# Kernel optimization log

Measured on AMD Instinct MI355X. Metric: run time of the kernel, lower is better.

## Reference

```python
import jax, jax.numpy as jnp
import numpy as np

N, D_IN, D_H, D_OUT = 65536, 256, 256, 128
E, TOP_K = 16, 2


def setup_inputs() -> dict:
    key = jax.random.key(0)
    ks = jax.random.split(key, 16)
    s = 0.05
    inp = {
        'x': jax.random.normal(ks[0], (N, D_IN), jnp.float32),
        'W0': jax.random.normal(ks[1], (D_IN, D_H), jnp.float32) * s,
        'b0': jnp.zeros((D_H,), jnp.float32),
        'Wg1': jax.random.normal(ks[2], (D_H, E), jnp.float32) * s,
        'bg1': jnp.zeros((E,), jnp.float32),
        'We1': jax.random.normal(ks[3], (E, D_H, D_H), jnp.float32) * s,
        'be1': jnp.zeros((E, D_H), jnp.float32),
        'Wg2': jax.random.normal(ks[4], (D_H, E), jnp.float32) * s,
        'bg2': jnp.zeros((E,), jnp.float32),
        'We2': jax.random.normal(ks[5], (E, D_H, D_H), jnp.float32) * s,
        'be2': jnp.zeros((E, D_H), jnp.float32),
        'Wf': jax.random.normal(ks[6], (D_H, D_OUT), jnp.float32) * s,
        'bf': jnp.zeros((D_OUT,), jnp.float32),
    }
    return inp


def _moe_layer(h, Wg, bg, We, be):
    # naive gate: logits over experts, top-k, renormalized softmax of top-k vals
    logits = h @ Wg + bg                      # [N, E]
    gate_full = jax.nn.softmax(logits, axis=-1)  # returned 'gate' for std stat
    vals, idx = jax.lax.top_k(logits, TOP_K)  # [N, k]
    scores = jax.nn.softmax(vals, axis=-1)    # [N, k]
    # scatter top-k scores into dense combine weights [N, E]
    cw = (jax.nn.one_hot(idx, E, dtype=h.dtype) * scores[..., None]).sum(axis=1)
    # grouped GEMM expressed as masked per-expert GEMMs (E is small, fixed)
    y = jnp.zeros((h.shape[0], We.shape[-1]), h.dtype)
    for e in range(E):
        y = y + cw[:, e:e + 1] * (h @ We[e] + be[e])
    # torch.std defaults to unbiased (ddof=1)
    gate_std_mean = jnp.std(gate_full, axis=1, ddof=1).mean()
    return y, gate_std_mean


def reference(x, W0, b0, Wg1, bg1, We1, be1, Wg2, bg2, We2, be2, Wf, bf):
    h = jax.nn.relu(x @ W0 + b0)
    h, g1 = _moe_layer(h, Wg1, bg1, We1, be1)
    h = jax.nn.relu(h)
    h, g2 = _moe_layer(h, Wg2, bg2, We2, be2)
    h = jax.nn.relu(h)
    out = h @ Wf + bf
    gate_std_means_mean = (g1 + g2) * 0.5
    return out, gate_std_means_mean
```

## Files before the change

kernel.cpp:

```cpp
#include <hip/hip_runtime.h>
#include <math.h>

#define NT 65536
#define DH 256
#define DO 128
#define NE 16

struct RInfo { int e1, e2; float s1, s2; };

typedef __attribute__((ext_vector_type(8))) short bh8;
typedef __attribute__((ext_vector_type(4))) float fx4;

static __device__ __forceinline__ short f2bf(float f) {
    union { float f; unsigned u; } v; v.f = f;
    return (short)((v.u + 0x7FFFu + ((v.u >> 16) & 1u)) >> 16);
}

template<bool RELU>
__global__ __launch_bounds__(256)
void gemm_dense(const float* __restrict__ A, const float* __restrict__ B,
                const float* __restrict__ bias, float* __restrict__ C,
                int ncols)
{
    __shared__ float As[128][24];
    __shared__ float Bs[16][132];
    const int tid = threadIdx.x;
    const int tx = tid & 15, ty = tid >> 4;
    const int rowBase = blockIdx.x * 128;
    const int colBase = blockIdx.y * 128;

    const int ra0 = tid >> 2, ga = tid & 3;
    const int kb0 = tid >> 5, cb = tid & 31;

    float acc[8][8];
#pragma unroll
    for (int i = 0; i < 8; ++i)
#pragma unroll
        for (int j = 0; j < 8; ++j) acc[i][j] = 0.f;

    for (int kt = 0; kt < DH; kt += 16) {
        *reinterpret_cast<float4*>(&As[ra0][ga * 4]) =
            *reinterpret_cast<const float4*>(&A[(size_t)(rowBase + ra0) * DH + kt + ga * 4]);
        *reinterpret_cast<float4*>(&As[ra0 + 64][ga * 4]) =
            *reinterpret_cast<const float4*>(&A[(size_t)(rowBase + ra0 + 64) * DH + kt + ga * 4]);
        *reinterpret_cast<float4*>(&Bs[kb0][cb * 4]) =
            *reinterpret_cast<const float4*>(&B[(size_t)(kt + kb0) * ncols + colBase + cb * 4]);
        *reinterpret_cast<float4*>(&Bs[kb0 + 8][cb * 4]) =
            *reinterpret_cast<const float4*>(&B[(size_t)(kt + kb0 + 8) * ncols + colBase + cb * 4]);
        __syncthreads();
#pragma unroll
        for (int k4 = 0; k4 < 16; k4 += 4) {
            alignas(16) float ar[8][4];
#pragma unroll
            for (int i = 0; i < 8; ++i)
                *reinterpret_cast<float4*>(ar[i]) =
                    *reinterpret_cast<const float4*>(&As[ty * 8 + i][k4]);
#pragma unroll
            for (int kk = 0; kk < 4; ++kk) {
                alignas(16) float br[8];
                *reinterpret_cast<float4*>(&br[0]) =
                    *reinterpret_cast<const float4*>(&Bs[k4 + kk][tx * 8]);
                *reinterpret_cast<float4*>(&br[4]) =
                    *reinterpret_cast<const float4*>(&Bs[k4 + kk][tx * 8 + 4]);
#pragma unroll
                for (int i = 0; i < 8; ++i) {
                    const float a = ar[i][kk];
#pragma unroll
                    for (int j = 0; j < 8; ++j)
                        acc[i][j] = fmaf(a, br[j], acc[i][j]);
                }
            }
        }
        __syncthreads();
    }
    alignas(16) float bb[8];
#pragma unroll
    for (int j = 0; j < 8; ++j) bb[j] = bias[colBase + tx * 8 + j];
#pragma unroll
    for (int i = 0; i < 8; ++i) {
        const size_t row = rowBase + ty * 8 + i;
        alignas(16) float o[8];
#pragma unroll
        for (int j = 0; j < 8; ++j) {
            float v = acc[i][j] + bb[j];
            if (RELU) v = fmaxf(v, 0.f);
            o[j] = v;
        }
        float* p = &C[row * (size_t)ncols + colBase + tx * 8];
        *reinterpret_cast<float4*>(p)     = *reinterpret_cast<float4*>(&o[0]);
        *reinterpret_cast<float4*>(p + 4) = *reinterpret_cast<float4*>(&o[4]);
    }
}

__global__ __launch_bounds__(256)
void gate_kernel(const float* __restrict__ H, const float* __restrict__ Wg,
                 const float* __restrict__ bg, RInfo* __restrict__ info,
                 float* gsum)
{
    __shared__ float wgs[256][17];
    __shared__ float hs[16][260];
    __shared__ float lg[16][17];
    __shared__ float sbg[16];
    __shared__ float sds[16];
    const int tid = threadIdx.x;
    const int rowBase = blockIdx.x * 16;

#pragma unroll
    for (int i = 0; i < 16; ++i) {
        const int idx = tid + 256 * i;
        wgs[idx >> 4][idx & 15] = Wg[idx];
    }
    if (tid < 16) sbg[tid] = bg[tid];
#pragma unroll
    for (int it = 0; it < 4; ++it) {
        const int flat = (tid + 256 * it) * 4;
        const int r = flat >> 8, k = flat & 255;
        *reinterpret_cast<float4*>(&hs[r][k]) =
            *reinterpret_cast<const float4*>(&H[(size_t)(rowBase + r) * DH + k]);
    }
    __syncthreads();
    {
        const int r = tid >> 4, e = tid & 15;
        float acc = 0.f;
#pragma unroll 8
        for (int k = 0; k < 256; ++k) acc = fmaf(hs[r][k], wgs[k][e], acc);
        lg[r][e] = acc + sbg[e];
    }
    __syncthreads();
    if (tid < 16) {
        const int row = rowBase + tid;
        float l[16];
#pragma unroll
        for (int i = 0; i < 16; ++i) l[i] = lg[tid][i];
        int i1 = 0; float v1 = l[0];
#pragma unroll
        for (int i = 1; i < 16; ++i) if (l[i] > v1) { v1 = l[i]; i1 = i; }
        int i2 = -1; float v2 = -INFINITY;
#pragma unroll
        for (int i = 0; i < 16; ++i) if (i != i1 && l[i] > v2) { v2 = l[i]; i2 = i; }
        const float t = expf(v2 - v1);
        const float s1 = 1.f / (1.f + t);
        const float s2 = t / (1.f + t);
        float p[16]; float S = 0.f;
#pragma unroll
        for (int i = 0; i < 16; ++i) { p[i] = expf(l[i] - v1); S += p[i]; }
        const float inv = 1.f / S;
        float sq = 0.f;
#pragma unroll
        for (int i = 0; i < 16; ++i) { const float q = p[i] * inv; sq = fmaf(q, q, sq); }
        const float var = (sq - 1.0f / 16.0f) * (1.0f / 15.0f);
        const float sd = sqrtf(fmaxf(var, 0.f));

        RInfo ri; ri.e1 = i1; ri.e2 = i2; ri.s1 = s1; ri.s2 = s2;
        info[row] = ri;
        sds[tid] = sd;
    }
    __syncthreads();
    if (tid == 0) {
        float s = 0.f;
#pragma unroll
        for (int i = 0; i < 16; ++i) s += sds[i];
        atomicAdd(gsum, s);
    }
}

__global__ void zero_gsum(float* gsum)
{
    if (threadIdx.x < 2) gsum[threadIdx.x] = 0.f;
}

__global__ __launch_bounds__(256)
void count_kernel(const RInfo* __restrict__ info, int* __restrict__ bc0,
                  int* __restrict__ bc1)
{
    __shared__ int h0[NE], h1[NE];
    const int tid = threadIdx.x, b = blockIdx.x;
    if (tid < NE) { h0[tid] = 0; h1[tid] = 0; }
    __syncthreads();
    const RInfo ri = info[b * 256 + tid];
    atomicAdd(&h0[ri.e1], 1);
    atomicAdd(&h1[ri.e2], 1);
    __syncthreads();
    if (tid < NE) {
        bc0[tid * 256 + b] = h0[tid];
        bc1[tid * 256 + b] = h1[tid];
    }
}

__global__ void scan2_kernel(const int* __restrict__ bc0, const int* __restrict__ bc1,
                             int* cnt0, int* cnt1, int* off0, int* off1,
                             int* __restrict__ bo0, int* __restrict__ bo1)
{
    __shared__ int tot0[NE], tot1[NE], base0[NE], base1[NE];
    const int t = threadIdx.x;
    if (t < NE) {
        int s = 0;
        for (int b = 0; b < 256; ++b) s += bc0[t * 256 + b];
        tot0[t] = s; cnt0[t] = s;
    } else if (t < 2 * NE) {
        const int e = t - NE;
        int s = 0;
        for (int b = 0; b < 256; ++b) s += bc1[e * 256 + b];
        tot1[e] = s; cnt1[e] = s;
    }
    __syncthreads();
    if (t == 0) { int a = 0; for (int e = 0; e < NE; ++e) { base0[e] = a; off0[e] = a; a += tot0[e]; } }
    if (t == 1) { int a = 0; for (int e = 0; e < NE; ++e) { base1[e] = a; off1[e] = a; a += tot1[e]; } }
    __syncthreads();
    if (t < NE) {
        int run = base0[t];
        for (int b = 0; b < 256; ++b) { bo0[t * 256 + b] = run; run += bc0[t * 256 + b]; }
    } else if (t < 2 * NE) {
        const int e = t - NE;
        int run = base1[e];
        for (int b = 0; b < 256; ++b) { bo1[e * 256 + b] = run; run += bc1[e * 256 + b]; }
    }
}

__global__ __launch_bounds__(256)
void scatter2_kernel(const RInfo* __restrict__ info, const int* __restrict__ bo0,
                     const int* __restrict__ bo1, int* __restrict__ l0,
                     int* __restrict__ l1)
{
    __shared__ int h0[NE], h1[NE];
    const int tid = threadIdx.x, b = blockIdx.x;
    if (tid < NE) { h0[tid] = 0; h1[tid] = 0; }
    __syncthreads();
    const int r = b * 256 + tid;
    const RInfo ri = info[r];
    const int p0 = atomicAdd(&h0[ri.e1], 1);
    const int p1 = atomicAdd(&h1[ri.e2], 1);
    l0[bo0[ri.e1 * 256 + b] + p0] = r;
    l1[bo1[ri.e2 * 256 + b] + p1] = r;
}

template<int SLOT>
__global__ __launch_bounds__(256)
void gemm_expert(const float* __restrict__ Hin, const float* __restrict__ We,
                 const float* __restrict__ be, const RInfo* __restrict__ info,
                 const int* __restrict__ list, const int* __restrict__ cnts,
                 const int* __restrict__ offs, float* __restrict__ P,
                 short* __restrict__ Ybf)
{
    __shared__ float As[128][24];
    __shared__ float Bs[16][132];
    __shared__ int   rs[128];
    __shared__ float ss[128];

    int c = blockIdx.x, e;
    int cnt = 0;
    for (e = 0; e < NE; ++e) {
        cnt = cnts[e];
        const int nch = (cnt + 127) >> 7;
        if (c < nch) break;
        c -= nch;
    }
    if (e >= NE) return;
    const int m = min(128, cnt - c * 128);
    const int base = offs[e] + c * 128;
    const int tid = threadIdx.x;
    const int tx = tid & 15, ty = tid >> 4;
    const int colBase = blockIdx.y * 128;

    if (tid < 128) {
        const int g = list[base + min(tid, m - 1)];
        rs[tid] = g;
        const RInfo ri = info[g];
        ss[tid] = (SLOT == 0) ? ri.s1 : ri.s2;
    }
    __syncthreads();

    const float* B = We + (size_t)e * DH * DH;
    const int ra0 = tid >> 2, ga = tid & 3;
    const int kb0 = tid >> 5, cb = tid & 31;
    const size_t arow0 = (size_t)rs[ra0] * DH;
    const size_t arow1 = (size_t)rs[ra0 + 64] * DH;

    float acc[8][8];
#pragma unroll
    for (int i = 0; i < 8; ++i)
#pragma unroll
        for (int j = 0; j < 8; ++j) acc[i][j] = 0.f;

    for (int kt = 0; kt < DH; kt += 16) {
        *reinterpret_cast<float4*>(&As[ra0][ga * 4]) =
            *reinterpret_cast<const float4*>(&Hin[arow0 + kt + ga * 4]);
        *reinterpret_cast<float4*>(&As[ra0 + 64][ga * 4]) =
            *reinterpret_cast<const float4*>(&Hin[arow1 + kt + ga * 4]);
        *reinterpret_cast<float4*>(&Bs[kb0][cb * 4]) =
            *reinterpret_cast<const float4*>(&B[(size_t)(kt + kb0) * DH + colBase + cb * 4]);
        *reinterpret_cast<float4*>(&Bs[kb0 + 8][cb * 4]) =
            *reinterpret_cast<const float4*>(&B[(size_t)(kt + kb0 + 8) * DH + colBase + cb * 4]);
        __syncthreads();
#pragma unroll
        for (int k4 = 0; k4 < 16; k4 += 4) {
            alignas(16) float ar[8][4];
#pragma unroll
            for (int i = 0; i < 8; ++i)
                *reinterpret_cast<float4*>(ar[i]) =
                    *reinterpret_cast<const float4*>(&As[ty * 8 + i][k4]);
#pragma unroll
            for (int kk = 0; kk < 4; ++kk) {
                alignas(16) float br[8];
                *reinterpret_cast<float4*>(&br[0]) =
                    *reinterpret_cast<const float4*>(&Bs[k4 + kk][tx * 8]);
                *reinterpret_cast<float4*>(&br[4]) =
                    *reinterpret_cast<const float4*>(&Bs[k4 + kk][tx * 8 + 4]);
#pragma unroll
                for (int i = 0; i < 8; ++i) {
                    const float a = ar[i][kk];
#pragma unroll
                    for (int j = 0; j < 8; ++j)
                        acc[i][j] = fmaf(a, br[j], acc[i][j]);
                }
            }
        }
        __syncthreads();
    }

    alignas(16) float bb[8];
#pragma unroll
    for (int j = 0; j < 8; ++j) bb[j] = be[(size_t)e * DH + colBase + tx * 8 + j];
#pragma unroll
    for (int i = 0; i < 8; ++i) {
        const int rl = ty * 8 + i;
        if (rl < m) {
            const int g = rs[rl];
            const float s = ss[rl];
            alignas(16) float o[8];
#pragma unroll
            for (int j = 0; j < 8; ++j) o[j] = s * (acc[i][j] + bb[j]);
            float* pp = &P[(size_t)g * DH + colBase + tx * 8];
            if (SLOT == 0) {
                *reinterpret_cast<float4*>(pp)     = *reinterpret_cast<float4*>(&o[0]);
                *reinterpret_cast<float4*>(pp + 4) = *reinterpret_cast<float4*>(&o[4]);
            } else {
                const float4 p0 = *reinterpret_cast<const float4*>(pp);
                const float4 p1 = *reinterpret_cast<const float4*>(pp + 4);
                alignas(16) float h[8];
                h[0] = fmaxf(o[0] + p0.x, 0.f); h[1] = fmaxf(o[1] + p0.y, 0.f);
                h[2] = fmaxf(o[2] + p0.z, 0.f); h[3] = fmaxf(o[3] + p0.w, 0.f);
                h[4] = fmaxf(o[4] + p1.x, 0.f); h[5] = fmaxf(o[5] + p1.y, 0.f);
                h[6] = fmaxf(o[6] + p1.z, 0.f); h[7] = fmaxf(o[7] + p1.w, 0.f);
                *reinterpret_cast<float4*>(pp)     = *reinterpret_cast<float4*>(&h[0]);
                *reinterpret_cast<float4*>(pp + 4) = *reinterpret_cast<float4*>(&h[4]);
                if (Ybf) {
                    bh8 yb;
#pragma unroll
                    for (int j = 0; j < 8; ++j) yb[j] = f2bf(h[j]);
                    *reinterpret_cast<bh8*>(&Ybf[(size_t)g * DH + colBase + tx * 8]) = yb;
                }
            }
        }
    }
}

__global__ __launch_bounds__(256)
void transp_bf16(const float* __restrict__ W, short* __restrict__ WT,
                 int K, int N)
{
    __shared__ float t[32][33];
    const int k0 = blockIdx.x * 32, n0 = blockIdx.y * 32;
    const size_t off = (size_t)blockIdx.z * K * N;
    const int c = threadIdx.x & 31, r8 = threadIdx.x >> 5;
#pragma unroll
    for (int it = 0; it < 4; ++it) {
        const int r = r8 + it * 8;
        t[r][c] = W[off + (size_t)(k0 + r) * N + n0 + c];
    }
    __syncthreads();
#pragma unroll
    for (int it = 0; it < 4; ++it) {
        const int r = r8 + it * 8;
        WT[off + (size_t)(n0 + r) * K + k0 + c] = f2bf(t[c][r]);
    }
}

template<int SLOT, int BFA>
__global__ __launch_bounds__(256)
void gemm_expert_bf16(const float* __restrict__ Yf, const short* __restrict__ Abf,
                      const short* __restrict__ WeT,
                      const float* __restrict__ be, const RInfo* __restrict__ info,
                      const int* __restrict__ list, const int* __restrict__ cnts,
                      const int* __restrict__ offs, float* __restrict__ P,
                      short* __restrict__ Hbf)
{
    __shared__ bh8 As8[512];
    __shared__ bh8 Bs8[512];
    __shared__ int   rs[128];
    __shared__ float ss[128];

    int c = blockIdx.x, e;
    int cnt = 0;
    for (e = 0; e < NE; ++e) {
        cnt = cnts[e];
        const int nch = (cnt + 127) >> 7;
        if (c < nch) break;
        c -= nch;
    }
    if (e >= NE) return;
    const int m = min(128, cnt - c * 128);
    const int base = offs[e] + c * 128;
    const int tid = threadIdx.x;

    if (tid < 128) {
        const int g = list[base + min(tid, m - 1)];
        rs[tid] = g;
        const RInfo ri = info[g];
        ss[tid] = (SLOT == 0) ? ri.s1 : ri.s2;
    }
    __syncthreads();

    const int colBase = blockIdx.y * 128;
    const int lane = tid & 63, wave = tid >> 6;
    const int wr = wave >> 1, wc = wave & 1;
    const short* Bw = WeT + (size_t)e * DH * DH;

    fx4 acc[4][4];
    const fx4 z = {0.f, 0.f, 0.f, 0.f};
#pragma unroll
    for (int i = 0; i < 4; ++i)
#pragma unroll
        for (int j = 0; j < 4; ++j) acc[i][j] = z;

    const int d0 = tid, d1 = tid + 256;
    const int ar0 = d0 >> 2, ak0 = d0 & 3;
    const int ar1 = d1 >> 2, ak1 = d1 & 3;
    const int g0 = ar0 * 4 + (ak0 ^ ((ar0 >> 1) & 3));
    const int g1 = ar1 * 4 + (ak1 ^ ((ar1 >> 1) & 3));
    const size_t arow0 = (size_t)rs[ar0] * DH, arow1 = (size_t)rs[ar1] * DH;
    const size_t brow0 = (size_t)(colBase + ar0) * DH, brow1 = (size_t)(colBase + ar1) * DH;

    for (int kt = 0; kt < DH; kt += 32) {
        if (BFA) {
            As8[g0] = *reinterpret_cast<const bh8*>(&Abf[arow0 + kt + ak0 * 8]);
            As8[g1] = *reinterpret_cast<const bh8*>(&Abf[arow1 + kt + ak1 * 8]);
        } else {
            const float* s0 = &Yf[arow0 + kt + ak0 * 8];
            const float4 f0 = *reinterpret_cast<const float4*>(s0);
            const float4 f1 = *reinterpret_cast<const float4*>(s0 + 4);
            bh8 v;
            v[0]=f2bf(f0.x); v[1]=f2bf(f0.y); v[2]=f2bf(f0.z); v[3]=f2bf(f0.w);
            v[4]=f2bf(f1.x); v[5]=f2bf(f1.y); v[6]=f2bf(f1.z); v[7]=f2bf(f1.w);
            As8[g0] = v;
            const float* s1 = &Yf[arow1 + kt + ak1 * 8];
            const float4 f2 = *reinterpret_cast<const float4*>(s1);
            const float4 f3 = *reinterpret_cast<const float4*>(s1 + 4);
            bh8 w;
            w[0]=f2bf(f2.x); w[1]=f2bf(f2.y); w[2]=f2bf(f2.z); w[3]=f2bf(f2.w);
            w[4]=f2bf(f3.x); w[5]=f2bf(f3.y); w[6]=f2bf(f3.z); w[7]=f2bf(f3.w);
            As8[g1] = w;
        }
        {
            Bs8[g0] = *reinterpret_cast<const bh8*>(&Bw[brow0 + kt + ak0 * 8]);
            Bs8[g1] = *reinterpret_cast<const bh8*>(&Bw[brow1 + kt + ak1 * 8]);
        }
        __syncthreads();
        const int kq = lane >> 4, lm = lane & 15;
        bh8 af[4], bfr[4];
#pragma unroll
        for (int i = 0; i < 4; ++i) {
            const int rl = wr * 64 + i * 16 + lm;
            af[i] = As8[rl * 4 + (kq ^ ((rl >> 1) & 3))];
            const int cl = wc * 64 + i * 16 + lm;
            bfr[i] = Bs8[cl * 4 + (kq ^ ((cl >> 1) & 3))];
        }
#pragma unroll
        for (int i = 0; i < 4; ++i)
#pragma unroll
            for (int j = 0; j < 4; ++j)
                acc[i][j] = __builtin_amdgcn_mfma_f32_16x16x32_bf16(
                    af[i], bfr[j], acc[i][j], 0, 0, 0);
        __syncthreads();
    }

    const int rq = lane >> 4, lm = lane & 15;
#pragma unroll
    for (int i = 0; i < 4; ++i) {
#pragma unroll
        for (int j = 0; j < 4; ++j) {
            const int rl = wr * 64 + i * 16 + rq * 4 + j;
            if (rl < m) {
                const int g = rs[rl];
                const float s = ss[rl];
#pragma unroll
                for (int nf = 0; nf < 4; ++nf) {
                    const int cl = colBase + wc * 64 + nf * 16 + lm;
                    float* pp = &P[(size_t)g * DH + cl];
                    const float o = s * (acc[i][nf][j] + be[(size_t)e * DH + cl]);
                    if (SLOT == 0) {
                        *pp = o;
                    } else {
                        const float v = fmaxf(*pp + o, 0.f);
                        if (BFA) Hbf[(size_t)g * DH + cl] = f2bf(v);
                        else     *pp = v;
                    }
                }
            }
        }
    }
}

template<int BFA>
__global__ __launch_bounds__(256)
void gemm_final_bf16(const float* __restrict__ Hf, const short* __restrict__ Habf,
                     const short* __restrict__ WT,
                     const float* __restrict__ bias, float* __restrict__ C,
                     const float* gsum, float* scalar_out)
{
    __shared__ bh8 As8[512];
    __shared__ bh8 Bs8[512];
    const int tid = threadIdx.x;
    const int rowBase = blockIdx.x * 128;

    if (blockIdx.x == 0 && tid == 0)
        *scalar_out = (gsum[0] + gsum[1]) * (0.5f / (float)NT);

    const int lane = tid & 63, wave = tid >> 6;
    const int wr = wave >> 1, wc = wave & 1;

    fx4 acc[4][4];
    const fx4 z = {0.f, 0.f, 0.f, 0.f};
#pragma unroll
    for (int i = 0; i < 4; ++i)
#pragma unroll
        for (int j = 0; j < 4; ++j) acc[i][j] = z;

    const int d0 = tid, d1 = tid + 256;
    const int ar0 = d0 >> 2, ak0 = d0 & 3;
    const int ar1 = d1 >> 2, ak1 = d1 & 3;
    const int g0 = ar0 * 4 + (ak0 ^ ((ar0 >> 1) & 3));
    const int g1 = ar1 * 4 + (ak1 ^ ((ar1 >> 1) & 3));
    const size_t arow0 = (size_t)(rowBase + ar0) * DH, arow1 = (size_t)(rowBase + ar1) * DH;
    const size_t brow0 = (size_t)ar0 * DH, brow1 = (size_t)ar1 * DH;

    for (int kt = 0; kt < DH; kt += 32) {
        if (BFA) {
            As8[g0] = *reinterpret_cast<const bh8*>(&Habf[arow0 + kt + ak0 * 8]);
            As8[g1] = *reinterpret_cast<const bh8*>(&Habf[arow1 + kt + ak1 * 8]);
        } else {
            const float* s0 = &Hf[arow0 + kt + ak0 * 8];
            const float4 f0 = *reinterpret_cast<const float4*>(s0);
            const float4 f1 = *reinterpret_cast<const float4*>(s0 + 4);
            bh8 v;
            v[0]=f2bf(f0.x); v[1]=f2bf(f0.y); v[2]=f2bf(f0.z); v[3]=f2bf(f0.w);
            v[4]=f2bf(f1.x); v[5]=f2bf(f1.y); v[6]=f2bf(f1.z); v[7]=f2bf(f1.w);
            As8[g0] = v;
            const float* s1 = &Hf[arow1 + kt + ak1 * 8];
            const float4 f2 = *reinterpret_cast<const float4*>(s1);
            const float4 f3 = *reinterpret_cast<const float4*>(s1 + 4);
            bh8 w;
            w[0]=f2bf(f2.x); w[1]=f2bf(f2.y); w[2]=f2bf(f2.z); w[3]=f2bf(f2.w);
            w[4]=f2bf(f3.x); w[5]=f2bf(f3.y); w[6]=f2bf(f3.z); w[7]=f2bf(f3.w);
            As8[g1] = w;
        }
        {
            Bs8[g0] = *reinterpret_cast<const bh8*>(&WT[brow0 + kt + ak0 * 8]);
            Bs8[g1] = *reinterpret_cast<const bh8*>(&WT[brow1 + kt + ak1 * 8]);
        }
        __syncthreads();
        const int kq = lane >> 4, lm = lane & 15;
        bh8 af[4], bfr[4];
#pragma unroll
        for (int i = 0; i < 4; ++i) {
            const int rl = wr * 64 + i * 16 + lm;
            af[i] = As8[rl * 4 + (kq ^ ((rl >> 1) & 3))];
            const int cl = wc * 64 + i * 16 + lm;
            bfr[i] = Bs8[cl * 4 + (kq ^ ((cl >> 1) & 3))];
        }
#pragma unroll
        for (int i = 0; i < 4; ++i)
#pragma unroll
            for (int j = 0; j < 4; ++j)
                acc[i][j] = __builtin_amdgcn_mfma_f32_16x16x32_bf16(
                    af[i], bfr[j], acc[i][j], 0, 0, 0);
        __syncthreads();
    }

    const int rq = lane >> 4, lm = lane & 15;
#pragma unroll
    for (int i = 0; i < 4; ++i) {
#pragma unroll
        for (int j = 0; j < 4; ++j) {
            const int rl = rowBase + wr * 64 + i * 16 + rq * 4 + j;
#pragma unroll
            for (int nf = 0; nf < 4; ++nf) {
                const int cl = wc * 64 + nf * 16 + lm;
                C[(size_t)rl * DO + cl] = acc[i][nf][j] + bias[cl];
            }
        }
    }
}

extern "C" void kernel_launch(void* const* d_in, const int* in_sizes, int n_in,
                              void* d_out, int out_size, void* d_ws, size_t ws_size,
                              hipStream_t stream)
{
    const float* x   = (const float*)d_in[0];
    const float* W0  = (const float*)d_in[1];
    const float* b0  = (const float*)d_in[2];
    const float* Wg1 = (const float*)d_in[3];
    const float* bg1 = (const float*)d_in[4];
    const float* We1 = (const float*)d_in[5];
    const float* be1 = (const float*)d_in[6];
    const float* Wg2 = (const float*)d_in[7];
    const float* bg2 = (const float*)d_in[8];
    const float* We2 = (const float*)d_in[9];
    const float* be2 = (const float*)d_in[10];
    const float* Wf  = (const float*)d_in[11];
    const float* bf  = (const float*)d_in[12];
    float* out = (float*)d_out;

    char* w = (char*)d_ws;
    float* H    = (float*)w; w += (size_t)NT * DH * 4;
    float* Y    = (float*)w; w += (size_t)NT * DH * 4;
    RInfo* info = (RInfo*)w; w += (size_t)NT * sizeof(RInfo);
    int* l0   = (int*)w; w += (size_t)NT * 4;
    int* l1   = (int*)w; w += (size_t)NT * 4;
    int* bc0  = (int*)w; w += NE * 256 * 4;
    int* bc1  = (int*)w; w += NE * 256 * 4;
    int* bo0  = (int*)w; w += NE * 256 * 4;
    int* bo1  = (int*)w; w += NE * 256 * 4;
    int* cnt0 = (int*)w; w += 64;
    int* cnt1 = (int*)w; w += 64;
    int* off0 = (int*)w; w += 64;
    int* off1 = (int*)w; w += 64;
    float* gsum = (float*)w; w += 64;
    short* WeT = (short*)w; w += (size_t)NE * DH * DH * 2;
    short* WfT = (short*)w; w += (size_t)DH * DO * 2;
    short* Ybf = (short*)w; w += (size_t)NT * DH * 2;
    const bool roomy = (size_t)(w - (char*)d_ws) <= ws_size;
    short* Hbf = (short*)Y;

    const int MAXCH = NT / 128 + NE;

    zero_gsum<<<dim3(1), dim3(64), 0, stream>>>(gsum);
    transp_bf16<<<dim3(8, 8, 16), dim3(256), 0, stream>>>(We2, WeT, DH, DH);
    transp_bf16<<<dim3(8, 4, 1),  dim3(256), 0, stream>>>(Wf,  WfT, DH, DO);

    gemm_dense<true><<<dim3(NT / 128, 2), dim3(256), 0, stream>>>(x, W0, b0, H, DH);

    gate_kernel<<<dim3(NT / 16), dim3(256), 0, stream>>>(H, Wg1, bg1, info, &gsum[0]);
    count_kernel<<<dim3(NT / 256), dim3(256), 0, stream>>>(info, bc0, bc1);
    scan2_kernel<<<dim3(1), dim3(64), 0, stream>>>(bc0, bc1, cnt0, cnt1, off0, off1, bo0, bo1);
    scatter2_kernel<<<dim3(NT / 256), dim3(256), 0, stream>>>(info, bo0, bo1, l0, l1);
    gemm_expert<0><<<dim3(MAXCH, 2), dim3(256), 0, stream>>>(H, We1, be1, info, l0, cnt0, off0, Y, nullptr);
    gemm_expert<1><<<dim3(MAXCH, 2), dim3(256), 0, stream>>>(H, We1, be1, info, l1, cnt1, off1, Y,
                                                             roomy ? Ybf : nullptr);

    gate_kernel<<<dim3(NT / 16), dim3(256), 0, stream>>>(Y, Wg2, bg2, info, &gsum[1]);
    count_kernel<<<dim3(NT / 256), dim3(256), 0, stream>>>(info, bc0, bc1);
    scan2_kernel<<<dim3(1), dim3(64), 0, stream>>>(bc0, bc1, cnt0, cnt1, off0, off1, bo0, bo1);
    scatter2_kernel<<<dim3(NT / 256), dim3(256), 0, stream>>>(info, bo0, bo1, l0, l1);
    if (roomy) {
        gemm_expert_bf16<0,1><<<dim3(MAXCH, 2), dim3(256), 0, stream>>>(Y, Ybf, WeT, be2, info, l0, cnt0, off0, H, nullptr);
        gemm_expert_bf16<1,1><<<dim3(MAXCH, 2), dim3(256), 0, stream>>>(Y, Ybf, WeT, be2, info, l1, cnt1, off1, H, Hbf);
        gemm_final_bf16<1><<<dim3(NT / 128), dim3(256), 0, stream>>>(H, Hbf, WfT, bf, out, gsum, out + (size_t)NT * DO);
    } else {
        gemm_expert_bf16<0,0><<<dim3(MAXCH, 2), dim3(256), 0, stream>>>(Y, nullptr, WeT, be2, info, l0, cnt0, off0, H, nullptr);
        gemm_expert_bf16<1,0><<<dim3(MAXCH, 2), dim3(256), 0, stream>>>(Y, nullptr, WeT, be2, info, l1, cnt1, off1, H, nullptr);
        gemm_final_bf16<0><<<dim3(NT / 128), dim3(256), 0, stream>>>(H, nullptr, WfT, bf, out, gsum, out + (size_t)NT * DO);
    }
}
```

Measured before the change: 630.0 us.

## Fuse expert counting into gate kernel, deepen fp32 GEMM K-tile, remap expert chunks

Folds the per-block expert histogram into the gate kernel using shared atomics plus global atomicAdd into zeroed bucket arrays. This removes the separate count kernel launch and its reread of routing info, and the scan kernel now re-zeros the buckets after use. The fp32 dense and expert GEMMs switch from a K-tile of 16 to 32, halving the number of barrier/load iterations at the cost of more shared memory. Expert GEMM blocks are remapped so that consecutive block IDs are strided across chunks (8 x 66), and the gate weight load is vectorised.

```diff
diff --git a/kernel.cpp b/kernel.cpp
--- a/kernel.cpp
+++ b/kernel.cpp
@@ -5,6 +5,8 @@
 #define DH 256
 #define DO 128
 #define NE 16
+#define MAXCH 528
+#define CPX 66
 
 struct RInfo { int e1, e2; float s1, s2; };
 
@@ -22,34 +24,41 @@
                 const float* __restrict__ bias, float* __restrict__ C,
                 int ncols)
 {
-    __shared__ float As[128][24];
-    __shared__ float Bs[16][132];
+    __shared__ float As[128][36];
+    __shared__ float Bs[32][132];
     const int tid = threadIdx.x;
     const int tx = tid & 15, ty = tid >> 4;
     const int rowBase = blockIdx.x * 128;
     const int colBase = blockIdx.y * 128;
 
-    const int ra0 = tid >> 2, ga = tid & 3;
-    const int kb0 = tid >> 5, cb = tid & 31;
-
     float acc[8][8];
 #pragma unroll
     for (int i = 0; i < 8; ++i)
 #pragma unroll
         for (int j = 0; j < 8; ++j) acc[i][j] = 0.f;
 
-    for (int kt = 0; kt < DH; kt += 16) {
-        *reinterpret_cast<float4*>(&As[ra0][ga * 4]) =
-            *reinterpret_cast<const float4*>(&A[(size_t)(rowBase + ra0) * DH + kt + ga * 4]);
-        *reinterpret_cast<float4*>(&As[ra0 + 64][ga * 4]) =
-            *reinterpret_cast<const float4*>(&A[(size_t)(rowBase + ra0 + 64) * DH + kt + ga * 4]);
-        *reinterpret_cast<float4*>(&Bs[kb0][cb * 4]) =
-            *reinterpret_cast<const float4*>(&B[(size_t)(kt + kb0) * ncols + colBase + cb * 4]);
-        *reinterpret_cast<float4*>(&Bs[kb0 + 8][cb * 4]) =
-            *reinterpret_cast<const float4*>(&B[(size_t)(kt + kb0 + 8) * ncols + colBase + cb * 4]);
-        __syncthreads();
-#pragma unroll
-        for (int k4 = 0; k4 < 16; k4 += 4) {
+    for (int kt = 0; kt < DH; kt += 32) {
+        {
+            const int r = tid >> 3, k4 = (tid & 7) << 2;
+#pragma unroll
+            for (int it = 0; it < 4; ++it) {
+                const float4 v = *reinterpret_cast<const float4*>(
+                    &A[(size_t)(rowBase + r + 32 * it) * DH + kt + k4]);
+                *reinterpret_cast<float4*>(&As[r + 32 * it][k4]) = v;
+            }
+        }
+        {
+            const int kr = tid >> 5, c4 = (tid & 31) << 2;
+#pragma unroll
+            for (int it = 0; it < 4; ++it) {
+                const float4 v = *reinterpret_cast<const float4*>(
+                    &B[(size_t)(kt + kr + 8 * it) * ncols + colBase + c4]);
+                *reinterpret_cast<float4*>(&Bs[kr + 8 * it][c4]) = v;
+            }
+        }
+        __syncthreads();
+#pragma unroll
+        for (int k4 = 0; k4 < 32; k4 += 4) {
             alignas(16) float ar[8][4];
 #pragma unroll
             for (int i = 0; i < 8; ++i)
@@ -95,22 +104,25 @@
 __global__ __launch_bounds__(256)
 void gate_kernel(const float* __restrict__ H, const float* __restrict__ Wg,
                  const float* __restrict__ bg, RInfo* __restrict__ info,
-                 float* gsum)
-{
-    __shared__ float wgs[256][17];
+                 float* gsum, int* __restrict__ bc0, int* __restrict__ bc1)
+{
+    __shared__ float wgs[256][20];
     __shared__ float hs[16][260];
     __shared__ float lg[16][17];
     __shared__ float sbg[16];
     __shared__ float sds[16];
+    __shared__ int hh0[NE], hh1[NE];
     const int tid = threadIdx.x;
     const int rowBase = blockIdx.x * 16;
 
 #pragma unroll
-    for (int i = 0; i < 16; ++i) {
-        const int idx = tid + 256 * i;
-        wgs[idx >> 4][idx & 15] = Wg[idx];
-    }
-    if (tid < 16) sbg[tid] = bg[tid];
+    for (int it = 0; it < 4; ++it) {
+        const int flat = (tid + 256 * it) * 4;
+        const int k = flat >> 4, e4 = flat & 15;
+        *reinterpret_cast<float4*>(&wgs[k][e4]) =
+            *reinterpret_cast<const float4*>(&Wg[flat]);
+    }
+    if (tid < 16) { sbg[tid] = bg[tid]; hh0[tid] = 0; hh1[tid] = 0; }
 #pragma unroll
     for (int it = 0; it < 4; ++it) {
         const int flat = (tid + 256 * it) * 4;
@@ -154,6 +166,8 @@
         RInfo ri; ri.e1 = i1; ri.e2 = i2; ri.s1 = s1; ri.s2 = s2;
         info[row] = ri;
         sds[tid] = sd;
+        atomicAdd(&hh0[i1], 1);
+        atomicAdd(&hh1[i2], 1);
     }
     __syncthreads();
     if (tid == 0) {
@@ -162,32 +176,21 @@
         for (int i = 0; i < 16; ++i) s += sds[i];
         atomicAdd(gsum, s);
     }
-}
-
-__global__ void zero_gsum(float* gsum)
-{
-    if (threadIdx.x < 2) gsum[threadIdx.x] = 0.f;
-}
-
-__global__ __launch_bounds__(256)
-void count_kernel(const RInfo* __restrict__ info, int* __restrict__ bc0,
-                  int* __restrict__ bc1)
-{
-    __shared__ int h0[NE], h1[NE];
-    const int tid = threadIdx.x, b = blockIdx.x;
-    if (tid < NE) { h0[tid] = 0; h1[tid] = 0; }
-    __syncthreads();
-    const RInfo ri = info[b * 256 + tid];
-    atomicAdd(&h0[ri.e1], 1);
-    atomicAdd(&h1[ri.e2], 1);
-    __syncthreads();
-    if (tid < NE) {
-        bc0[tid * 256 + b] = h0[tid];
-        bc1[tid * 256 + b] = h1[tid];
-    }
-}
-
-__global__ void scan2_kernel(const int* __restrict__ bc0, const int* __restrict__ bc1,
+    if (tid < 16) {
+        const int b = blockIdx.x >> 4;
+        if (hh0[tid]) atomicAdd(&bc0[tid * 256 + b], hh0[tid]);
+        if (hh1[tid]) atomicAdd(&bc1[tid * 256 + b], hh1[tid]);
+    }
+}
+
+__global__ void zero_meta(int* bc0, int* bc1, float* gsum)
+{
+    const int idx = blockIdx.x * 256 + threadIdx.x;
+    bc0[idx] = 0; bc1[idx] = 0;
+    if (idx < 2) gsum[idx] = 0.f;
+}
+
+__global__ void scan2_kernel(int* __restrict__ bc0, int* __restrict__ bc1,
                              int* cnt0, int* cnt1, int* off0, int* off1,
                              int* __restrict__ bo0, int* __restrict__ bo1)
 {
@@ -215,6 +218,8 @@
         int run = base1[e];
         for (int b = 0; b < 256; ++b) { bo1[e * 256 + b] = run; run += bc1[e * 256 + b]; }
     }
+    __syncthreads();
+    for (int i = t; i < NE * 256; i += 64) { bc0[i] = 0; bc1[i] = 0; }
 }
 
 __global__ __launch_bounds__(256)
@@ -242,12 +247,13 @@
                  const int* __restrict__ offs, float* __restrict__ P,
                  short* __restrict__ Ybf)
 {
-    __shared__ float As[128][24];
-    __shared__ float Bs[16][132];
+    __shared__ float As[128][36];
+    __shared__ float Bs[32][132];
     __shared__ int   rs[128];
     __shared__ float ss[128];
 
-    int c = blockIdx.x, e;
+    int c = (blockIdx.x & 7) * CPX + (blockIdx.x >> 3);
+    int e;
     int cnt = 0;
     for (e = 0; e < NE; ++e) {
         cnt = cnts[e];
@@ -271,10 +277,6 @@
     __syncthreads();
 
     const float* B = We + (size_t)e * DH * DH;
-    const int ra0 = tid >> 2, ga = tid & 3;
-    const int kb0 = tid >> 5, cb = tid & 31;
-    const size_t arow0 = (size_t)rs[ra0] * DH;
-    const size_t arow1 = (size_t)rs[ra0 + 64] * DH;
 
     float acc[8][8];
 #pragma unroll
@@ -282,18 +284,29 @@
 #pragma unroll
         for (int j = 0; j < 8; ++j) acc[i][j] = 0.f;
 
-    for (int kt = 0; kt < DH; kt += 16) {
-        *reinterpret_cast<float4*>(&As[ra0][ga * 4]) =
-            *reinterpret_cast<const float4*>(&Hin[arow0 + kt + ga * 4]);
-        *reinterpret_cast<float4*>(&As[ra0 + 64][ga * 4]) =
-            *reinterpret_cast<const float4*>(&Hin[arow1 + kt + ga * 4]);
-        *reinterpret_cast<float4*>(&Bs[kb0][cb * 4]) =
-            *reinterpret_cast<const float4*>(&B[(size_t)(kt + kb0) * DH + colBase + cb * 4]);
-        *reinterpret_cast<float4*>(&Bs[kb0 + 8][cb * 4]) =
-            *reinterpret_cast<const float4*>(&B[(size_t)(kt + kb0 + 8) * DH + colBase + cb * 4]);
-        __syncthreads();
-#pragma unroll
-        for (int k4 = 0; k4 < 16; k4 += 4) {
+    for (int kt = 0; kt < DH; kt += 32) {
+        {
+            const int r = tid >> 3, k4 = (tid & 7) << 2;
+#pragma unroll
+            for (int it = 0; it < 4; ++it) {
+                const int g = rs[r + 32 * it];
+                const float4 v = *reinterpret_cast<const float4*>(
+                    &Hin[(size_t)g * DH + kt + k4]);
+                *reinterpret_cast<float4*>(&As[r + 32 * it][k4]) = v;
+            }
+        }
+        {
+            const int kr = tid >> 5, c4 = (tid & 31) << 2;
+#pragma unroll
+            for (int it = 0; it < 4; ++it) {
+                const float4 v = *reinterpret_cast<const float4*>(
+                    &B[(size_t)(kt + kr + 8 * it) * DH + colBase + c4]);
+                *reinterpret_cast<float4*>(&Bs[kr + 8 * it][c4]) = v;
+            }
+        }
+        __syncthreads();
+#pragma unroll
+        for (int k4 = 0; k4 < 32; k4 += 4) {
             alignas(16) float ar[8][4];
 #pragma unroll
             for (int i = 0; i < 8; ++i)
@@ -390,7 +403,8 @@
     __shared__ int   rs[128];
     __shared__ float ss[128];
 
-    int c = blockIdx.x, e;
+    int c = (blockIdx.x & 7) * CPX + (blockIdx.x >> 3);
+    int e;
     int cnt = 0;
     for (e = 0; e < NE; ++e) {
         cnt = cnts[e];
@@ -632,24 +646,20 @@
     const bool roomy = (size_t)(w - (char*)d_ws) <= ws_size;
     short* Hbf = (short*)Y;
 
-    const int MAXCH = NT / 128 + NE;
-
-    zero_gsum<<<dim3(1), dim3(64), 0, stream>>>(gsum);
+    zero_meta<<<dim3(16), dim3(256), 0, stream>>>(bc0, bc1, gsum);
     transp_bf16<<<dim3(8, 8, 16), dim3(256), 0, stream>>>(We2, WeT, DH, DH);
     transp_bf16<<<dim3(8, 4, 1),  dim3(256), 0, stream>>>(Wf,  WfT, DH, DO);
 
     gemm_dense<true><<<dim3(NT / 128, 2), dim3(256), 0, stream>>>(x, W0, b0, H, DH);
 
-    gate_kernel<<<dim3(NT / 16), dim3(256), 0, stream>>>(H, Wg1, bg1, info, &gsum[0]);
-    count_kernel<<<dim3(NT / 256), dim3(256), 0, stream>>>(info, bc0, bc1);
+    gate_kernel<<<dim3(NT / 16), dim3(256), 0, stream>>>(H, Wg1, bg1, info, &gsum[0], bc0, bc1);
     scan2_kernel<<<dim3(1), dim3(64), 0, stream>>>(bc0, bc1, cnt0, cnt1, off0, off1, bo0, bo1);
     scatter2_kernel<<<dim3(NT / 256), dim3(256), 0, stream>>>(info, bo0, bo1, l0, l1);
     gemm_expert<0><<<dim3(MAXCH, 2), dim3(256), 0, stream>>>(H, We1, be1, info, l0, cnt0, off0, Y, nullptr);
     gemm_expert<1><<<dim3(MAXCH, 2), dim3(256), 0, stream>>>(H, We1, be1, info, l1, cnt1, off1, Y,
                                                              roomy ? Ybf : nullptr);
 
-    gate_kernel<<<dim3(NT / 16), dim3(256), 0, stream>>>(Y, Wg2, bg2, info, &gsum[1]);
-    count_kernel<<<dim3(NT / 256), dim3(256), 0, stream>>>(info, bc0, bc1);
+    gate_kernel<<<dim3(NT / 16), dim3(256), 0, stream>>>(Y, Wg2, bg2, info, &gsum[1], bc0, bc1);
     scan2_kernel<<<dim3(1), dim3(64), 0, stream>>>(bc0, bc1, cnt0, cnt1, off0, off1, bo0, bo1);
     scatter2_kernel<<<dim3(NT / 256), dim3(256), 0, stream>>>(info, bo0, bo1, l0, l1);
     if (roomy) {
```

Measured after the change: 610.9 us. 1.03x faster.
